# Optimization experiments

Measured on AMD Instinct MI355X. Metric: run time of the kernel, lower is better.

## Reference

```python
import jax, jax.numpy as jnp
import numpy as np

B, S, D = 32, 257, 1024
H, HD = 16, 64
E, R, K = 8, 16, 2
SCALE = HD ** -0.5


def _lora_linear(x, w_fixed, A_all, B_all, bias, idx, gates):
    # x: [B,S,D]; w_fixed: [O,D]; A_all: [E,R,D]; B_all: [E,O,R]; idx: [B,K]; gates: [B,K]
    base = jnp.einsum('bsd,od->bso', x, w_fixed)
    A_sel = A_all[idx]  # [B,K,R,D] per-sample expert gather
    B_sel = B_all[idx]  # [B,K,O,R]
    xa = jnp.einsum('bsd,bkrd->bksr', x, A_sel)          # low-rank down-proj
    expert = jnp.einsum('bksr,bkor,bk->bso', xa, B_sel, gates)
    return base + expert + bias


def setup_inputs() -> dict:
    key = jax.random.key(0)
    ks = jax.random.split(key, 20)
    inp = {
        'hidden_states': jax.random.normal(ks[0], (B, S, D), jnp.float32),
        'top_k_indices': jax.random.randint(ks[1], (B, K), 0, E),
        'top_k_gates': jax.random.uniform(ks[2], (B, K), jnp.float32),
    }
    i = 3
    for name in ('q', 'k', 'v', 'o'):
        inp[f'w{name}_fixed'] = jax.random.normal(ks[i], (D, D), jnp.float32) * 0.02; i += 1
        inp[f'A_{name}'] = jax.random.normal(ks[i], (E, R, D), jnp.float32) * 0.02; i += 1
        inp[f'B_{name}'] = jax.random.normal(ks[i], (E, D, R), jnp.float32) * 0.02; i += 1
        inp[f'b_{name}'] = jnp.zeros((D,), jnp.float32)
    return inp


def reference(hidden_states, top_k_indices, top_k_gates,
              wq_fixed, A_q, B_q, b_q,
              wk_fixed, A_k, B_k, b_k,
              wv_fixed, A_v, B_v, b_v,
              wo_fixed, A_o, B_o, b_o):
    idx, gates = top_k_indices, top_k_gates
    q = _lora_linear(hidden_states, wq_fixed, A_q, B_q, b_q, idx, gates) * SCALE
    k = _lora_linear(hidden_states, wk_fixed, A_k, B_k, b_k, idx, gates)
    v = _lora_linear(hidden_states, wv_fixed, A_v, B_v, b_v, idx, gates)
    # [B,S,D] -> [B,H,S,HD]
    q = q.reshape(B, S, H, HD).transpose(0, 2, 1, 3)
    k = k.reshape(B, S, H, HD).transpose(0, 2, 1, 3)
    v = v.reshape(B, S, H, HD).transpose(0, 2, 1, 3)
    attn = jax.nn.softmax(jnp.einsum('bhsd,bhtd->bhst', q, k), axis=-1)
    out = jnp.einsum('bhst,bhtd->bhsd', attn, v)
    out = out.transpose(0, 2, 1, 3).reshape(B, S, D)
    return _lora_linear(out, wo_fixed, A_o, B_o, b_o, idx, gates)
```

## Files before the change

kernel.cpp:

```cpp
#include <hip/hip_runtime.h>


#define BB 32
#define SS 257
#define DD 1024
#define HH 16
#define HDIM 64
#define EE 8
#define RR 16
#define MTOT (BB * SS)
#define MPAD 8448
#define VTS 264

typedef __attribute__((ext_vector_type(8))) _Float16 f16x8;
typedef __attribute__((ext_vector_type(4))) float f32x4;

static __device__ __forceinline__ float4 ld4(const float* p) {
    return *(const float4*)p;
}
static __device__ __forceinline__ unsigned short f16b(float x) {
    union { _Float16 f; unsigned short u; } cv;
    cv.f = (_Float16)x;
    return cv.u;
}

static __device__ __forceinline__ void gl_lds16(const unsigned short* g,
                                                unsigned short* l) {
    __builtin_amdgcn_global_load_lds(
        (const __attribute__((address_space(1))) unsigned int*)g,
        (__attribute__((address_space(3))) unsigned int*)l, 16, 0, 0);
}

static __device__ __forceinline__ int xcd_swz(int orig, int nwg) {
    const int xcd = orig & 7;
    const int lin = orig >> 3;
    const int q = nwg >> 3;
    const int r = nwg & 7;
    return (xcd < r ? xcd * (q + 1) : r * (q + 1) + (xcd - r) * q) + lin;
}

__global__ __launch_bounds__(256) void prep(
    const float* __restrict__ hidden, const float* __restrict__ wq,
    const float* __restrict__ wk, const float* __restrict__ wv,
    const float* __restrict__ wo, const float* __restrict__ Aq,
    const float* __restrict__ Ak, const float* __restrict__ Av,
    const float* __restrict__ Ao, const float* __restrict__ Bq,
    const float* __restrict__ Bk, const float* __restrict__ Bv,
    const float* __restrict__ Bo, const int* __restrict__ tki,
    const float* __restrict__ tkg, unsigned short* __restrict__ Xf,
    unsigned short* __restrict__ Wcat, unsigned short* __restrict__ Who,
    unsigned short* __restrict__ A3, unsigned short* __restrict__ Ao16,
    unsigned short* __restrict__ Bccat, unsigned short* __restrict__ Bco)
{
    const int tid = threadIdx.x;
    int bx = blockIdx.x;
    if (bx < 8448) {
        long i = ((long)bx * 256 + tid) * 4;
        float4 v = (i < (long)MTOT * DD) ? ld4(&hidden[i])
                                         : make_float4(0.f, 0.f, 0.f, 0.f);
        ushort4 hv;
        hv.x = f16b(v.x); hv.y = f16b(v.y); hv.z = f16b(v.z); hv.w = f16b(v.w);
        *(ushort4*)&Xf[i] = hv;
        return;
    }
    bx -= 8448;
    if (bx < 4096) {
        const int sel = bx >> 10;
        long i = ((long)(bx & 1023) * 256 + tid) * 4;
        const float* src = (sel == 0) ? wq : (sel == 1) ? wk
                                          : (sel == 2) ? wv : wo;
        unsigned short* dst =
            (sel < 3) ? Wcat + (size_t)sel * DD * DD : Who;
        float4 v = ld4(&src[i]);
        ushort4 hv;
        hv.x = f16b(v.x); hv.y = f16b(v.y); hv.z = f16b(v.z); hv.w = f16b(v.w);
        *(ushort4*)&dst[i] = hv;
        return;
    }
    bx -= 4096;
    if (bx < 512) {
        const int sel = bx >> 7;
        long i = ((long)(bx & 127) * 256 + tid) * 4;
        const float* src = (sel == 0) ? Aq : (sel == 1) ? Ak
                                          : (sel == 2) ? Av : Ao;
        unsigned short* dst =
            (sel < 3) ? A3 + (size_t)sel * EE * RR * DD : Ao16;
        float4 v = ld4(&src[i]);
        ushort4 hv;
        hv.x = f16b(v.x); hv.y = f16b(v.y); hv.z = f16b(v.z); hv.w = f16b(v.w);
        *(ushort4*)&dst[i] = hv;
        return;
    }
    bx -= 512;
    {
        const int set = bx >> 8;
        const int i = (bx & 255) * 256 + tid;
        const int b = i >> 11;
        const int rem = i & 2047;
        const int n = rem >> 1;
        const int ke = rem & 1;
        const float* Ball = (set == 0) ? Bq : (set == 1) ? Bk
                                           : (set == 2) ? Bv : Bo;
        const int e = tki[b * 2 + ke];
        const float g = tkg[b * 2 + ke];
        const float* sp = &Ball[((size_t)e * DD + n) * RR];
        unsigned short o16[16];
#pragma unroll
        for (int r4 = 0; r4 < 4; ++r4) {
            float4 v = ld4(sp + r4 * 4);
            o16[r4 * 4 + 0] = f16b(g * v.x);
            o16[r4 * 4 + 1] = f16b(g * v.y);
            o16[r4 * 4 + 2] = f16b(g * v.z);
            o16[r4 * 4 + 3] = f16b(g * v.w);
        }
        unsigned short* dst =
            (set < 3) ? &Bccat[((size_t)b * 3072 + set * 1024 + n) * 32 + ke * 16]
                      : &Bco[((size_t)b * 1024 + n) * 32 + ke * 16];
        *(uint4*)&dst[0] = *(uint4*)&o16[0];
        *(uint4*)&dst[8] = *(uint4*)&o16[8];
    }
}

#define COMPUTE1()                                                             \
    do {                                                                       \
        f16x8 af[4], bf[4];                                                    \
        const int sb = (quad ^ ((l16 >> 1) & 3)) * 8;                          \
        _Pragma("unroll") for (int t = 0; t < 4; ++t) {                        \
            af[t] = *(const f16x8*)&Ah[(wm + t * 16 + l16) * 32 + sb];         \
            bf[t] = *(const f16x8*)&Bh[(wn + t * 16 + l16) * 32 + sb];         \
        }                                                                      \
        _Pragma("unroll") for (int i = 0; i < 4; ++i)                          \
        _Pragma("unroll") for (int j = 0; j < 4; ++j)                          \
            acc[i][j] = __builtin_amdgcn_mfma_f32_16x16x32_f16(                \
                af[i], bf[j], acc[i][j], 0, 0, 0);                             \
    } while (0)

__global__ __launch_bounds__(256) void gemm_xa(
    const unsigned short* __restrict__ Xf, const unsigned short* __restrict__ A0,
    const unsigned short* __restrict__ A1, const unsigned short* __restrict__ A2,
    unsigned short* __restrict__ XA, int ncols)
{
    __shared__ unsigned short Ah[128 * 32];
    __shared__ unsigned short Bh[128 * 32];
    const int tid = threadIdx.x;
    const int m0 = blockIdx.y * 128;
    const int p = blockIdx.x;
    const unsigned short* Ap = (p == 0) ? A0 : (p == 1) ? A1 : A2;
    const int lane = tid & 63;
    const int w = tid >> 6;
    const int wm = (w >> 1) * 64;
    const int wn = (w & 1) * 64;
    const int l16 = lane & 15;
    const int quad = lane >> 4;

    f32x4 acc[4][4];
#pragma unroll
    for (int i = 0; i < 4; ++i)
#pragma unroll
        for (int j = 0; j < 4; ++j) acc[i][j] = (f32x4){0.f, 0.f, 0.f, 0.f};

    const int srow = tid >> 2;
    const int scol = (((tid & 3) ^ ((tid >> 3) & 3))) * 8;
    const int lbase = (tid & 192) * 8;
    const size_t xr0 = (size_t)(m0 + srow) * DD + scol;
    const size_t xr1 = (size_t)(m0 + srow + 64) * DD + scol;
    const size_t ar0 = (size_t)srow * DD + scol;
    const size_t ar1 = (size_t)(srow + 64) * DD + scol;

#pragma unroll 1
    for (int kt = 0; kt < 32; ++kt) {
        const int k0 = kt * 32;
        gl_lds16(Xf + xr0 + k0, &Ah[lbase]);
        gl_lds16(Xf + xr1 + k0, &Ah[2048 + lbase]);
        gl_lds16(Ap + ar0 + k0, &Bh[lbase]);
        gl_lds16(Ap + ar1 + k0, &Bh[2048 + lbase]);
        __syncthreads();
        COMPUTE1();
        __syncthreads();
    }

#pragma unroll
    for (int j = 0; j < 4; ++j) {
        const int col = p * 128 + wn + j * 16 + l16;
#pragma unroll
        for (int i = 0; i < 4; ++i) {
            const int mb = m0 + wm + i * 16 + quad * 4;
#pragma unroll
            for (int rg = 0; rg < 4; ++rg) {
                const int m = mb + rg;
                if (m < MTOT)
                    XA[(size_t)m * ncols + col] = f16b(acc[i][j][rg]);
            }
        }
    }
}

#define QKV_STAGE(BUFI, KT)                                                    \
    do {                                                                       \
        unsigned short* dA_ = S + (BUFI) * 16384 + w * 512;                    \
        const int k0_ = (KT) * 32;                                             \
        gl_lds16(Xf + gA + k0_, dA_);                                          \
        gl_lds16(Wcat + gB + k0_, dA_ + 8192);                                 \
    } while (0)

#define QKV_PHASES(BUFI)                                                       \
    do {                                                                       \
        const unsigned short* Ab_ = S + (BUFI) * 16384;                        \
        const unsigned short* Bb_ = Ab_ + 8192;                                \
        f16x8 af_[4], bf_[4];                                                  \
        _Pragma("unroll") for (int j = 0; j < 4; ++j)                          \
            bf_[j] = *(const f16x8*)&Bb_[boff + j * 512];                      \
        _Pragma("unroll") for (int i = 0; i < 4; ++i)                          \
            af_[i] = *(const f16x8*)&Ab_[aoff + i * 512];                      \
        __builtin_amdgcn_s_setprio(1);                                         \
        _Pragma("unroll") for (int i = 0; i < 4; ++i)                          \
        _Pragma("unroll") for (int j = 0; j < 4; ++j)                          \
            acc[i][j] = __builtin_amdgcn_mfma_f32_16x16x32_f16(                \
                af_[i], bf_[j], acc[i][j], 0, 0, 0);                           \
        __builtin_amdgcn_s_setprio(0);                                         \
    } while (0)

#define QKV_SYNC() asm volatile("s_waitcnt vmcnt(0)\n\ts_barrier" ::: "memory")

#define QKV_MAIN_LOOP()                                                        \
    do {                                                                       \
        QKV_STAGE(0, 0);                                                       \
        QKV_STAGE(1, 1);                                                       \
        QKV_SYNC();                                                            \
        _Pragma("unroll 1") for (int qq = 0; qq < 8; ++qq) {                   \
            const int kb_ = qq * 4;                                            \
            if (kb_ + 2 < 32) {                                                \
                QKV_STAGE(2, kb_ + 2);                                         \
                QKV_STAGE(3, kb_ + 3);                                         \
            }                                                                  \
            QKV_PHASES(0);                                                     \
            QKV_PHASES(1);                                                     \
            QKV_SYNC();                                                        \
            if (kb_ + 4 < 32) {                                                \
                QKV_STAGE(0, kb_ + 4);                                         \
                QKV_STAGE(1, kb_ + 5);                                         \
            }                                                                  \
            QKV_PHASES(2);                                                     \
            QKV_PHASES(3);                                                     \
            QKV_SYNC();                                                        \
        }                                                                      \
    } while (0)

__global__ __launch_bounds__(1024)
__attribute__((amdgpu_waves_per_eu(4, 8))) void gemm_qkv(
    const unsigned short* __restrict__ Xf, const unsigned short* __restrict__ Wcat,
    const float* __restrict__ bq, const float* __restrict__ bk,
    const float* __restrict__ bv, const unsigned short* __restrict__ XAd,
    const unsigned short* __restrict__ Bccat, const int* __restrict__ idx,
    unsigned short* __restrict__ qh, unsigned short* __restrict__ kh,
    unsigned short* __restrict__ vTg)
{
    __shared__ unsigned short S[32768];
    const int tid = threadIdx.x;
    const int wgid = xcd_swz(blockIdx.x, 396);
    const int bxn = wgid % 12;
    const int m0 = (wgid / 12) * 256;
    const int p = bxn >> 2;
    const int n0g = bxn * 256;
    const int nloc0 = (bxn & 3) * 256;
    const int lane = tid & 63;
    const int w = tid >> 6;
    const int wm = (w >> 2) * 64;
    const int wn = (w & 3) * 64;
    const int l16 = lane & 15;
    const int quad = lane >> 4;
    const int sb = (quad ^ ((l16 >> 1) & 3)) * 8;
    const int aoff = (wm + l16) * 32 + sb;
    const int boff = (wn + l16) * 32 + sb;

    f32x4 acc[4][4];
#pragma unroll
    for (int i = 0; i < 4; ++i)
#pragma unroll
        for (int j = 0; j < 4; ++j) acc[i][j] = (f32x4){0.f, 0.f, 0.f, 0.f};

    const int srow = tid >> 2;
    const int schk = ((tid & 3) ^ ((srow >> 1) & 3)) * 8;
    const size_t gA = (size_t)(m0 + srow) * DD + schk;
    const size_t gB = (size_t)(n0g + srow) * DD + schk;

    QKV_STAGE(0, 0);
#pragma unroll 1
    for (int kt = 0; kt < 32; ++kt) {
        QKV_SYNC();
        if (kt < 31) QKV_STAGE((kt + 1) & 1, kt + 1);
        QKV_PHASES(kt & 1);
    }

    {
        int m_hi = m0 + 255;
        if (m_hi >= MTOT) m_hi = MTOT - 1;
        const int b_first = m0 / SS;
        const int b_last = m_hi / SS;
        const int r = tid >> 2;
        const int cc = tid & 3;
        const int key = (r >> 1) & 3;
        const int g = cc ^ key;
        const uint4 z = make_uint4(0, 0, 0, 0);
#pragma unroll 1
        for (int bp = b_first; bp <= b_last; ++bp) {
            const int gm = m0 + r;
            const bool va = (gm < MTOT) && (gm / SS == bp);
            uint4 av = z;
            if (va) {
                const int e = idx[bp * 2 + (g >> 1)];
                av = *(const uint4*)&XAd[(size_t)gm * 384 + p * 128 +
                                         e * 16 + (g & 1) * 8];
            }
            const size_t bo = ((size_t)bp * 3072 + p * 1024 + nloc0 + r) * 32;
            uint4 bv2 = *(const uint4*)&Bccat[bo + g * 8];
            __syncthreads();
            *(uint4*)&S[r * 32 + cc * 8] = av;
            *(uint4*)&S[8192 + r * 32 + cc * 8] = bv2;
            __syncthreads();
            QKV_PHASES(0);
            __syncthreads();
        }
    }

    unsigned short* Epi = S;
    const float* bias = (p == 0) ? bq : (p == 1) ? bk : bv;
    if (p < 2) {
        const float alpha = (p == 0) ? 0.125f : 1.0f;
        unsigned short* C = (p == 0) ? qh : kh;
#pragma unroll 1
        for (int qtr = 0; qtr < 4; ++qtr) {
            if ((w >> 2) == qtr) {
#pragma unroll
                for (int j = 0; j < 4; ++j) {
                    const int col = wn + j * 16 + l16;
                    const float bvl = bias[nloc0 + col];
#pragma unroll
                    for (int i = 0; i < 4; ++i) {
                        const int ml = i * 16 + quad * 4;
#pragma unroll
                        for (int rg = 0; rg < 4; ++rg)
                            Epi[(ml + rg) * 264 + col] =
                                f16b(alpha * (acc[i][j][rg] + bvl));
                    }
                }
            }
            __syncthreads();
            {
                const int r = tid >> 4;
                const int c = (tid & 15) * 16;
                const int m = m0 + qtr * 64 + r;
                if (m < MTOT) {
#pragma unroll
                    for (int k = 0; k < 2; ++k)
                        *(uint4*)&C[(size_t)m * DD + nloc0 + c + k * 8] =
                            *(const uint4*)&Epi[r * 264 + c + k * 8];
                }
            }
            __syncthreads();
        }
    } else {
#pragma unroll 1
        for (int hh = 0; hh < 4; ++hh) {
            if ((w >> 2) == hh) {
#pragma unroll
                for (int j = 0; j < 4; ++j) {
                    const int col = wn + j * 16 + l16;
                    const float bvl = bias[nloc0 + col];
#pragma unroll
                    for (int i = 0; i < 4; ++i) {
                        const int ml = i * 16 + quad * 4;
                        ushort4 pk;
                        pk.x = f16b(acc[i][j][0] + bvl);
                        pk.y = f16b(acc[i][j][1] + bvl);
                        pk.z = f16b(acc[i][j][2] + bvl);
                        pk.w = f16b(acc[i][j][3] + bvl);
                        *(ushort4*)&Epi[col * 68 + ml] = pk;
                    }
                }
            }
            __syncthreads();
            {
                const int tl = tid & 63;
                const int mg = m0 + hh * 64 + tl;
                if (mg < MTOT) {
                    const int bq2 = mg / SS;
                    const int t = mg - bq2 * SS;
#pragma unroll 4
                    for (int k = 0; k < 16; ++k) {
                        const int nll = (tid >> 6) + k * 16;
                        const int d = nloc0 + nll;
                        vTg[((size_t)(bq2 * HH + (d >> 6)) * HDIM + (d & 63)) *
                                VTS + t] = Epi[nll * 68 + tl];
                    }
                }
            }
            __syncthreads();
        }
    }
}

__global__ __launch_bounds__(1024)
__attribute__((amdgpu_waves_per_eu(4, 4))) void gemm_o(
    const unsigned short* __restrict__ Xf, const unsigned short* __restrict__ Wh2,
    const float* __restrict__ bias, const unsigned short* __restrict__ XAo,
    const unsigned short* __restrict__ Bco, const int* __restrict__ idx,
    float* __restrict__ Cf)
{
    __shared__ unsigned short S[65536];
    const unsigned short* Wcat = Wh2;
    const int tid = threadIdx.x;
    const int wgid = xcd_swz(blockIdx.x, 132);
    const int m0 = (wgid / 4) * 256;
    const int n0 = (wgid % 4) * 256;
    const int lane = tid & 63;
    const int w = tid >> 6;
    const int wm = (w >> 2) * 64;
    const int wn = (w & 3) * 64;
    const int l16 = lane & 15;
    const int quad = lane >> 4;
    const int sb = (quad ^ ((l16 >> 1) & 3)) * 8;
    const int aoff = (wm + l16) * 32 + sb;
    const int boff = (wn + l16) * 32 + sb;

    f32x4 acc[4][4];
#pragma unroll
    for (int i = 0; i < 4; ++i)
#pragma unroll
        for (int j = 0; j < 4; ++j) acc[i][j] = (f32x4){0.f, 0.f, 0.f, 0.f};

    const int srow = tid >> 2;
    const int schk = ((tid & 3) ^ ((srow >> 1) & 3)) * 8;
    const size_t gA = (size_t)(m0 + srow) * DD + schk;
    const size_t gB = (size_t)(n0 + srow) * DD + schk;

    QKV_MAIN_LOOP();

    {
        int m_hi = m0 + 255;
        if (m_hi >= MTOT) m_hi = MTOT - 1;
        const int b_first = m0 / SS;
        const int b_last = m_hi / SS;
        const int r = tid >> 2;
        const int cc = tid & 3;
        const int key = (r >> 1) & 3;
        const int g = cc ^ key;
        const uint4 z = make_uint4(0, 0, 0, 0);
#pragma unroll 1
        for (int bp = b_first; bp <= b_last; ++bp) {
            const int gm = m0 + r;
            const bool va = (gm < MTOT) && (gm / SS == bp);
            uint4 av = z;
            if (va) {
                const int e = idx[bp * 2 + (g >> 1)];
                av = *(const uint4*)&XAo[(size_t)gm * 128 + e * 16 +
                                         (g & 1) * 8];
            }
            const size_t bo = ((size_t)bp * 1024 + n0 + r) * 32;
            uint4 bv2 = *(const uint4*)&Bco[bo + g * 8];
            __syncthreads();
            *(uint4*)&S[r * 32 + cc * 8] = av;
            *(uint4*)&S[8192 + r * 32 + cc * 8] = bv2;
            __syncthreads();
            QKV_PHASES(0);
            __syncthreads();
        }
    }

#pragma unroll
    for (int j = 0; j < 4; ++j) {
        const int n = n0 + wn + j * 16 + l16;
        const float bvl = bias[n];
#pragma unroll
        for (int i = 0; i < 4; ++i) {
            const int mb = m0 + wm + i * 16 + quad * 4;
#pragma unroll
            for (int rg = 0; rg < 4; ++rg) {
                const int m = mb + rg;
                if (m < MTOT) Cf[(size_t)m * DD + n] = acc[i][j][rg] + bvl;
            }
        }
    }
}

__global__ __launch_bounds__(512, 1) void attn_v4(
    const unsigned short* __restrict__ qh, const unsigned short* __restrict__ kh,
    const unsigned short* __restrict__ vT, unsigned short* __restrict__ Xf)
{
    __shared__ unsigned short Ks[288 * 64];
    __shared__ unsigned short Vt[64 * VTS];
    __shared__ unsigned short Qs[64 * 64];
    __shared__ unsigned short Ps[64 * 296];
    __shared__ float sredm[2][64];
    __shared__ float sreds[2][64];

    const int tid = threadIdx.x;
    const int h = blockIdx.x, b = blockIdx.y;
    const int cb = h * HDIM;
    const int lane = tid & 63;
    const int w = tid >> 6;
    const int r0 = (w & 3) * 16;
    const int ch = w >> 2;
    const int l16 = lane & 15;
    const int quad = lane >> 4;

    const size_t kbase = (size_t)(b * SS) * DD + cb;
    {
        const int rr = w * 8 + (lane >> 3);
        const int cg = ((lane & 7) ^ (rr & 7)) * 8;
#pragma unroll
        for (int c = 0; c < 4; ++c)
            gl_lds16(kh + kbase + (size_t)(c * 64 + rr) * DD + cg,
                     &Ks[(c * 64 + w * 8) * 64]);
    }
    if (tid < 256) {
        uint4 z = make_uint4(0, 0, 0, 0);
        if (tid < 8) z = *(const uint4*)&kh[kbase + (size_t)256 * DD + tid * 8];
        *(uint4*)&Ks[256 * 64 + tid * 8] = z;
    }
    {
        const size_t vbase = (size_t)(b * HH + h) * HDIM * VTS;
        for (int i = tid; i < 64 * 33; i += 512) {
            const int r = i / 33;
            const int c = i - r * 33;
            uint4 v = *(const uint4*)&vT[vbase + (size_t)r * VTS + c * 8];
            if (c == 32) { v.x &= 0xFFFFu; v.y = 0; v.z = 0; v.w = 0; }
            *(uint4*)&Vt[r * VTS + c * 8] = v;
        }
    }

#pragma unroll 1
    for (int qt = 0; qt < 5; ++qt) {
        const int s0 = qt * 64;
        __syncthreads();
        {
            int sg = s0 + (tid >> 3);
            if (sg > SS - 1) sg = SS - 1;
            const int cg = ((tid & 7) ^ ((tid >> 3) & 7)) * 8;
            gl_lds16(qh + (size_t)(b * SS + sg) * DD + cb + cg,
                     &Qs[(w * 8) * 64]);
        }
        __syncthreads();

        f32x4 lac[9];
#pragma unroll
        for (int ct = 0; ct < 9; ++ct) lac[ct] = (f32x4){0.f, 0.f, 0.f, 0.f};
#pragma unroll
        for (int kc = 0; kc < 2; ++kc) {
            const int sb = ((kc * 4 + quad) ^ (l16 & 7)) * 8;
            f16x8 af = *(const f16x8*)&Qs[(r0 + l16) * 64 + sb];
#pragma unroll
            for (int ct = 0; ct < 9; ++ct) {
                const int c0 = ch * 144 + ct * 16;
                f16x8 bf = *(const f16x8*)&Ks[(c0 + l16) * 64 + sb];
                lac[ct] = __builtin_amdgcn_mfma_f32_16x16x32_f16(
                    af, bf, lac[ct], 0, 0, 0);
            }
        }
#pragma unroll
        for (int ct = 0; ct < 9; ++ct) {
            const int t = ch * 144 + ct * 16 + l16;
            if (t > SS - 1) {
                lac[ct][0] = -1e30f; lac[ct][1] = -1e30f;
                lac[ct][2] = -1e30f; lac[ct][3] = -1e30f;
            }
        }
        float mx[4] = {-1e30f, -1e30f, -1e30f, -1e30f};
#pragma unroll
        for (int ct = 0; ct < 9; ++ct)
#pragma unroll
            for (int i = 0; i < 4; ++i) mx[i] = fmaxf(mx[i], lac[ct][i]);
#pragma unroll
        for (int o = 1; o < 16; o <<= 1)
#pragma unroll
            for (int i = 0; i < 4; ++i)
                mx[i] = fmaxf(mx[i], __shfl_xor(mx[i], o, 16));
        if (l16 == 0)
#pragma unroll
            for (int i = 0; i < 4; ++i) sredm[ch][r0 + quad * 4 + i] = mx[i];
        __syncthreads();
#pragma unroll
        for (int i = 0; i < 4; ++i)
            mx[i] = fmaxf(mx[i], sredm[1 - ch][r0 + quad * 4 + i]);
        float sm[4] = {0.f, 0.f, 0.f, 0.f};
#pragma unroll
        for (int ct = 0; ct < 9; ++ct)
#pragma unroll
            for (int i = 0; i < 4; ++i) {
                float pv = __expf(lac[ct][i] - mx[i]);
                lac[ct][i] = pv;
                sm[i] += pv;
            }
#pragma unroll
        for (int o = 1; o < 16; o <<= 1)
#pragma unroll
            for (int i = 0; i < 4; ++i) sm[i] += __shfl_xor(sm[i], o, 16);
        if (l16 == 0)
#pragma unroll
            for (int i = 0; i < 4; ++i) sreds[ch][r0 + quad * 4 + i] = sm[i];
        __syncthreads();
        float inv[4];
#pragma unroll
        for (int i = 0; i < 4; ++i)
            inv[i] = 1.f / (sm[i] + sreds[1 - ch][r0 + quad * 4 + i]);
#pragma unroll
        for (int ct = 0; ct < 9; ++ct) {
            const int col = ch * 144 + ct * 16 + l16;
#pragma unroll
            for (int i = 0; i < 4; ++i)
                Ps[(r0 + quad * 4 + i) * 296 + col] =
                    f16b(lac[ct][i] * inv[i]);
        }
        __syncthreads();

        f32x4 oacc[2];
        oacc[0] = (f32x4){0.f, 0.f, 0.f, 0.f};
        oacc[1] = (f32x4){0.f, 0.f, 0.f, 0.f};
#pragma unroll
        for (int tt = 0; tt < 9; ++tt) {
            const int t0 = tt * 32;
            f16x8 pf = *(const f16x8*)&Ps[(r0 + l16) * 296 + t0 + quad * 8];
#pragma unroll
            for (int dt = 0; dt < 2; ++dt) {
                f16x8 bvv = *(const f16x8*)&Vt[(ch * 32 + dt * 16 + l16) * VTS +
                                               t0 + quad * 8];
                oacc[dt] = __builtin_amdgcn_mfma_f32_16x16x32_f16(
                    pf, bvv, oacc[dt], 0, 0, 0);
            }
        }
#pragma unroll
        for (int dt = 0; dt < 2; ++dt)
#pragma unroll
            for (int i = 0; i < 4; ++i) {
                const int srow = s0 + r0 + quad * 4 + i;
                if (srow < SS)
                    Xf[(size_t)(b * SS + srow) * DD + cb + ch * 32 + dt * 16 +
                       l16] = f16b(oacc[dt][i]);
            }
    }
}

extern "C" void kernel_launch(void* const* d_in, const int* in_sizes, int n_in,
                              void* d_out, int out_size, void* d_ws,
                              size_t ws_size, hipStream_t stream)
{
    const float* hidden = (const float*)d_in[0];
    const int* tki = (const int*)d_in[1];
    const float* tkg = (const float*)d_in[2];
    const float* wq = (const float*)d_in[3];
    const float* Aq = (const float*)d_in[4];
    const float* Bq = (const float*)d_in[5];
    const float* bq = (const float*)d_in[6];
    const float* wk = (const float*)d_in[7];
    const float* Ak = (const float*)d_in[8];
    const float* Bk = (const float*)d_in[9];
    const float* bkb = (const float*)d_in[10];
    const float* wv = (const float*)d_in[11];
    const float* Av = (const float*)d_in[12];
    const float* Bv = (const float*)d_in[13];
    const float* bvb = (const float*)d_in[14];
    const float* wo = (const float*)d_in[15];
    const float* Ao = (const float*)d_in[16];
    const float* Bo = (const float*)d_in[17];
    const float* bob = (const float*)d_in[18];
    float* out = (float*)d_out;

    char* ws = (char*)d_ws;
    const size_t NW = (size_t)DD * DD;
    const size_t NA = (size_t)EE * RR * DD;
    unsigned short* Xf = (unsigned short*)ws;    ws += (size_t)MPAD * DD * 2;
    unsigned short* qh = (unsigned short*)ws;    ws += (size_t)MTOT * DD * 2;
    unsigned short* vTg = (unsigned short*)ws;   ws += (size_t)BB * HH * HDIM * VTS * 2;
    unsigned short* Wcat = (unsigned short*)ws;  ws += 3 * NW * 2;
    unsigned short* Who = (unsigned short*)ws;   ws += NW * 2;
    unsigned short* A3 = (unsigned short*)ws;    ws += 3 * NA * 2;
    unsigned short* Ao16 = (unsigned short*)ws;  ws += NA * 2;
    unsigned short* Bccat = (unsigned short*)ws; ws += (size_t)BB * 3072 * 32 * 2;
    unsigned short* Bco = (unsigned short*)ws;   ws += (size_t)BB * 1024 * 32 * 2;
    unsigned short* XAo = (unsigned short*)ws;   ws += (size_t)MTOT * 128 * 2;
    unsigned short* kh = (unsigned short*)d_out;
    unsigned short* XAd = (unsigned short*)((char*)d_out + (size_t)MTOT * DD * 2);

    prep<<<14080, 256, 0, stream>>>(hidden, wq, wk, wv, wo, Aq, Ak, Av, Ao,
                                    Bq, Bk, Bv, Bo, tki, tkg, Xf, Wcat, Who,
                                    A3, Ao16, Bccat, Bco);
    gemm_xa<<<dim3(3, 65), 256, 0, stream>>>(Xf, A3, A3 + NA, A3 + 2 * NA,
                                             XAd, 384);
    gemm_qkv<<<396, 1024, 0, stream>>>(Xf, Wcat, bq, bkb, bvb, XAd,
                                       Bccat, tki, qh, kh, vTg);
    attn_v4<<<dim3(HH, BB), 512, 0, stream>>>(qh, kh, vTg, Xf);
    gemm_xa<<<dim3(1, 65), 256, 0, stream>>>(Xf, Ao16, Ao16, Ao16, XAo, 128);
    gemm_o<<<132, 1024, 0, stream>>>(Xf, Who, bob, XAo, Bco, tki, out);
}
```

Before: 335.0 us.

## Retile O-projection GEMM to 256x128 blocks with double-buffered K loop

The output-projection GEMM moves from 132 workgroups of 1024 threads with 256x256 tiles and a four-buffer pipeline to 264 workgroups of 512 threads with 256x128 tiles and a simpler two-buffer loop. This uses less LDS per workgroup and launches twice as many blocks, so the grid covers the CUs better and more than one workgroup can sit on a CU. In exchange, each block reuses fewer B tiles and the shallower prefetch may expose more memory latency. The low-rank expert epilogue staging is rewritten to fit the new thread count.

```diff
diff --git a/kernel.cpp b/kernel.cpp
--- a/kernel.cpp
+++ b/kernel.cpp
@@ -221,30 +221,6 @@
     } while (0)
 
 #define QKV_SYNC() asm volatile("s_waitcnt vmcnt(0)\n\ts_barrier" ::: "memory")
-
-#define QKV_MAIN_LOOP()                                                        \
-    do {                                                                       \
-        QKV_STAGE(0, 0);                                                       \
-        QKV_STAGE(1, 1);                                                       \
-        QKV_SYNC();                                                            \
-        _Pragma("unroll 1") for (int qq = 0; qq < 8; ++qq) {                   \
-            const int kb_ = qq * 4;                                            \
-            if (kb_ + 2 < 32) {                                                \
-                QKV_STAGE(2, kb_ + 2);                                         \
-                QKV_STAGE(3, kb_ + 3);                                         \
-            }                                                                  \
-            QKV_PHASES(0);                                                     \
-            QKV_PHASES(1);                                                     \
-            QKV_SYNC();                                                        \
-            if (kb_ + 4 < 32) {                                                \
-                QKV_STAGE(0, kb_ + 4);                                         \
-                QKV_STAGE(1, kb_ + 5);                                         \
-            }                                                                  \
-            QKV_PHASES(2);                                                     \
-            QKV_PHASES(3);                                                     \
-            QKV_SYNC();                                                        \
-        }                                                                      \
-    } while (0)
 
 __global__ __launch_bounds__(1024)
 __attribute__((amdgpu_waves_per_eu(4, 8))) void gemm_qkv(
@@ -400,23 +376,48 @@
     }
 }
 
-__global__ __launch_bounds__(1024)
-__attribute__((amdgpu_waves_per_eu(4, 4))) void gemm_o(
+#define O_STAGE(BUFI, KT)                                                      \
+    do {                                                                       \
+        unsigned short* b_ = S + (BUFI) * 12288;                               \
+        const int k0_ = (KT) * 32;                                             \
+        gl_lds16(Xf + gA1 + k0_, b_ + w * 1024);                               \
+        gl_lds16(Xf + gA2 + k0_, b_ + w * 1024 + 512);                         \
+        gl_lds16(Wh2 + gB + k0_, b_ + 8192 + w * 512);                         \
+    } while (0)
+
+#define O_PHASES(BUFI)                                                         \
+    do {                                                                       \
+        const unsigned short* Ab_ = S + (BUFI) * 12288;                        \
+        const unsigned short* Bb_ = Ab_ + 8192;                                \
+        f16x8 af_[4], bf_[4];                                                  \
+        _Pragma("unroll") for (int j = 0; j < 4; ++j)                          \
+            bf_[j] = *(const f16x8*)&Bb_[boff + j * 512];                      \
+        _Pragma("unroll") for (int i = 0; i < 4; ++i)                          \
+            af_[i] = *(const f16x8*)&Ab_[aoff + i * 512];                      \
+        __builtin_amdgcn_s_setprio(1);                                         \
+        _Pragma("unroll") for (int i = 0; i < 4; ++i)                          \
+        _Pragma("unroll") for (int j = 0; j < 4; ++j)                          \
+            acc[i][j] = __builtin_amdgcn_mfma_f32_16x16x32_f16(                \
+                af_[i], bf_[j], acc[i][j], 0, 0, 0);                           \
+        __builtin_amdgcn_s_setprio(0);                                         \
+    } while (0)
+
+__global__ __launch_bounds__(512)
+__attribute__((amdgpu_waves_per_eu(2, 8))) void gemm_o(
     const unsigned short* __restrict__ Xf, const unsigned short* __restrict__ Wh2,
     const float* __restrict__ bias, const unsigned short* __restrict__ XAo,
     const unsigned short* __restrict__ Bco, const int* __restrict__ idx,
     float* __restrict__ Cf)
 {
-    __shared__ unsigned short S[65536];
-    const unsigned short* Wcat = Wh2;
+    __shared__ unsigned short S[24576];
     const int tid = threadIdx.x;
-    const int wgid = xcd_swz(blockIdx.x, 132);
-    const int m0 = (wgid / 4) * 256;
-    const int n0 = (wgid % 4) * 256;
+    const int wgid = xcd_swz(blockIdx.x, 264);
+    const int m0 = (wgid >> 3) * 256;
+    const int n0 = (wgid & 7) * 128;
     const int lane = tid & 63;
     const int w = tid >> 6;
-    const int wm = (w >> 2) * 64;
-    const int wn = (w & 3) * 64;
+    const int wm = (w >> 1) * 64;
+    const int wn = (w & 1) * 64;
     const int l16 = lane & 15;
     const int quad = lane >> 4;
     const int sb = (quad ^ ((l16 >> 1) & 3)) * 8;
@@ -429,40 +430,57 @@
 #pragma unroll
         for (int j = 0; j < 4; ++j) acc[i][j] = (f32x4){0.f, 0.f, 0.f, 0.f};
 
-    const int srow = tid >> 2;
-    const int schk = ((tid & 3) ^ ((srow >> 1) & 3)) * 8;
-    const size_t gA = (size_t)(m0 + srow) * DD + schk;
-    const size_t gB = (size_t)(n0 + srow) * DD + schk;
-
-    QKV_MAIN_LOOP();
+    const int rowA1 = w * 32 + (lane >> 2);
+    const int chk = lane & 3;
+    const int keyA = (rowA1 >> 1) & 3;
+    const size_t gA1 = (size_t)(m0 + rowA1) * DD + (chk ^ keyA) * 8;
+    const size_t gA2 = gA1 + (size_t)16 * DD;
+    const int rowB = w * 16 + (lane >> 2);
+    const int keyB = (rowB >> 1) & 3;
+    const size_t gB = (size_t)(n0 + rowB) * DD + (chk ^ keyB) * 8;
+
+    O_STAGE(0, 0);
+#pragma unroll 1
+    for (int kt = 0; kt < 32; ++kt) {
+        QKV_SYNC();
+        if (kt < 31) O_STAGE((kt + 1) & 1, kt + 1);
+        O_PHASES(kt & 1);
+    }
 
     {
         int m_hi = m0 + 255;
         if (m_hi >= MTOT) m_hi = MTOT - 1;
         const int b_first = m0 / SS;
         const int b_last = m_hi / SS;
-        const int r = tid >> 2;
-        const int cc = tid & 3;
-        const int key = (r >> 1) & 3;
-        const int g = cc ^ key;
+        const int rA = tid >> 1;
+        const int b0 = (tid & 1) * 2;
+        const int keyTA = (rA >> 1) & 3;
+        const int g0 = b0 ^ keyTA, g1 = (b0 + 1) ^ keyTA;
+        const int rB = tid >> 2;
+        const int ccB = tid & 3;
+        const int gBt = ccB ^ ((rB >> 1) & 3);
         const uint4 z = make_uint4(0, 0, 0, 0);
 #pragma unroll 1
         for (int bp = b_first; bp <= b_last; ++bp) {
-            const int gm = m0 + r;
+            const int gm = m0 + rA;
             const bool va = (gm < MTOT) && (gm / SS == bp);
-            uint4 av = z;
+            uint4 av0 = z, av1 = z;
             if (va) {
-                const int e = idx[bp * 2 + (g >> 1)];
-                av = *(const uint4*)&XAo[(size_t)gm * 128 + e * 16 +
-                                         (g & 1) * 8];
-            }
-            const size_t bo = ((size_t)bp * 1024 + n0 + r) * 32;
-            uint4 bv2 = *(const uint4*)&Bco[bo + g * 8];
-            __syncthreads();
-            *(uint4*)&S[r * 32 + cc * 8] = av;
-            *(uint4*)&S[8192 + r * 32 + cc * 8] = bv2;
-            __syncthreads();
-            QKV_PHASES(0);
+                const int e0 = idx[bp * 2 + (g0 >> 1)];
+                const int e1 = idx[bp * 2 + (g1 >> 1)];
+                av0 = *(const uint4*)&XAo[(size_t)gm * 128 + e0 * 16 +
+                                          (g0 & 1) * 8];
+                av1 = *(const uint4*)&XAo[(size_t)gm * 128 + e1 * 16 +
+                                          (g1 & 1) * 8];
+            }
+            const size_t bo = ((size_t)bp * 1024 + n0 + rB) * 32;
+            uint4 bv2 = *(const uint4*)&Bco[bo + gBt * 8];
+            __syncthreads();
+            *(uint4*)&S[rA * 32 + b0 * 8] = av0;
+            *(uint4*)&S[rA * 32 + (b0 + 1) * 8] = av1;
+            *(uint4*)&S[8192 + rB * 32 + ccB * 8] = bv2;
+            __syncthreads();
+            O_PHASES(0);
             __syncthreads();
         }
     }
@@ -690,5 +708,5 @@
                                        Bccat, tki, qh, kh, vTg);
     attn_v4<<<dim3(HH, BB), 512, 0, stream>>>(qh, kh, vTg, Xf);
     gemm_xa<<<dim3(1, 65), 256, 0, stream>>>(Xf, Ao16, Ao16, Ao16, XAo, 128);
-    gemm_o<<<132, 1024, 0, stream>>>(Xf, Who, bob, XAo, Bco, tki, out);
-}
+    gemm_o<<<264, 512, 0, stream>>>(Xf, Who, bob, XAo, Bco, tki, out);
+}
```

Result: no change. 334.0 us (-0.3%).
